# Performance work log

Measured on AMD Instinct MI355X. Metric: run time of the kernel, lower is better.

## Reference

```python
import jax, jax.numpy as jnp
import numpy as np
from functools import partial

EPS = 1e-8

@partial(jax.custom_vjp, nondiff_argnums=(2, 3))
def ste_quantize(x, scale, clamp_min, clamp_max):
    # forward: clamp(round(x/scale), min, max); backward: grad/scale (STE)
    return jnp.clip(jnp.round(x / scale), clamp_min, clamp_max)

def _ste_fwd(x, scale, clamp_min, clamp_max):
    return ste_quantize(x, scale, clamp_min, clamp_max), scale

def _ste_bwd(clamp_min, clamp_max, scale, g):
    return (g / scale, jnp.zeros_like(scale))

ste_quantize.defvjp(_ste_fwd, _ste_bwd)


def setup_inputs() -> dict:
    key = jax.random.key(0)
    kx, kw = jax.random.split(key)
    x = jax.random.normal(kx, (4, 4096, 2048), dtype=jnp.float32)
    # nn.init.normal_(weight, mean=0.0, std=0.006)
    weight = 0.006 * jax.random.normal(kw, (2048, 2048), dtype=jnp.float32)
    return {"x": x, "weight": weight}


def reference(x, weight):
    # per-tensor ternary weight quantization: alpha = mean(|W|)
    alpha = jnp.maximum(jnp.mean(jnp.abs(weight)), EPS)
    w_q = ste_quantize(weight, alpha, -1.0, 1.0)  # (out, in), values in {-1,0,1}
    # per-token int8 activation quantization: beta = max(|x|)/127
    beta = jnp.maximum(jnp.max(jnp.abs(x), axis=-1, keepdims=True) / 127.0, EPS)  # (b,s,1)
    x_q = ste_quantize(x, beta, -127.0, 127.0)  # (b,s,in)
    # fp32 GEMM on quantized values, then dequant rescale
    y = jnp.einsum('bsi,oi->bso', x_q, w_q)
    return y * alpha * beta
```

## Files before the change

kernel.cpp:

```cpp
#include <hip/hip_runtime.h>

#define IN_DIM 2048
#define OUT_DIM 2048
#define EPS 1e-8f

#define BM 256
#define BN 128
#define BK 64
#define NT (IN_DIM / BK)
#define SLOT 24576
#define LDS_SZ 73728

using int32x4 = __attribute__((ext_vector_type(4))) int;

__global__ __launch_bounds__(256) void absum_kernel(const float* __restrict__ w,
                                                    double* __restrict__ sum, int n4) {
    int tid = blockIdx.x * blockDim.x + threadIdx.x;
    int stride = gridDim.x * blockDim.x;
    float s = 0.f;
    for (int i = tid; i < n4; i += stride) {
        float4 v = ((const float4*)w)[i];
        s += fabsf(v.x) + fabsf(v.y) + fabsf(v.z) + fabsf(v.w);
    }
    for (int off = 32; off; off >>= 1) s += __shfl_down(s, off);
    __shared__ float wsum[4];
    int lane = threadIdx.x & 63, wave = threadIdx.x >> 6;
    if (lane == 0) wsum[wave] = s;
    __syncthreads();
    if (threadIdx.x == 0) {
        double t = (double)wsum[0] + (double)wsum[1] + (double)wsum[2] + (double)wsum[3];
        atomicAdd(sum, t);
    }
}

__global__ __launch_bounds__(256) void quantw_kernel(const float* __restrict__ w,
                                                     const double* __restrict__ sumptr,
                                                     signed char* __restrict__ wq,
                                                     float* __restrict__ alpha_out, int n4) {
    float alpha = fmaxf((float)(*sumptr * (1.0 / (double)(IN_DIM * OUT_DIM))), EPS);
    int i = blockIdx.x * blockDim.x + threadIdx.x;
    if (i == 0) *alpha_out = alpha;
    if (i >= n4) return;
    float4 v = ((const float4*)w)[i];
    char4 q;
    q.x = (signed char)fminf(fmaxf(rintf(v.x / alpha), -1.f), 1.f);
    q.y = (signed char)fminf(fmaxf(rintf(v.y / alpha), -1.f), 1.f);
    q.z = (signed char)fminf(fmaxf(rintf(v.z / alpha), -1.f), 1.f);
    q.w = (signed char)fminf(fmaxf(rintf(v.w / alpha), -1.f), 1.f);
    ((char4*)wq)[i] = q;
}

__global__ __launch_bounds__(256) void quantx_kernel(const float* __restrict__ x,
                                                     signed char* __restrict__ xq,
                                                     float* __restrict__ beta_arr,
                                                     int tokens) {
    const int tid = threadIdx.x;
    const int lane = tid & 63, wave = tid >> 6;
    __shared__ float wmax[4];
    for (int t = blockIdx.x; t < tokens; t += gridDim.x) {
        const float4* row = (const float4*)(x + (size_t)t * IN_DIM);
        float4 v0 = row[tid];
        float4 v1 = row[tid + 256];
        float m = fmaxf(fmaxf(fmaxf(fabsf(v0.x), fabsf(v0.y)), fmaxf(fabsf(v0.z), fabsf(v0.w))),
                        fmaxf(fmaxf(fabsf(v1.x), fabsf(v1.y)), fmaxf(fabsf(v1.z), fabsf(v1.w))));
        for (int off = 32; off; off >>= 1) m = fmaxf(m, __shfl_xor(m, off));
        if (lane == 0) wmax[wave] = m;
        __syncthreads();
        m = fmaxf(fmaxf(wmax[0], wmax[1]), fmaxf(wmax[2], wmax[3]));
        float beta = fmaxf(m * (1.f / 127.f), EPS);
        if (tid == 0) beta_arr[t] = beta;
        char4 q0, q1;
        q0.x = (signed char)fminf(fmaxf(rintf(v0.x / beta), -127.f), 127.f);
        q0.y = (signed char)fminf(fmaxf(rintf(v0.y / beta), -127.f), 127.f);
        q0.z = (signed char)fminf(fmaxf(rintf(v0.z / beta), -127.f), 127.f);
        q0.w = (signed char)fminf(fmaxf(rintf(v0.w / beta), -127.f), 127.f);
        q1.x = (signed char)fminf(fmaxf(rintf(v1.x / beta), -127.f), 127.f);
        q1.y = (signed char)fminf(fmaxf(rintf(v1.y / beta), -127.f), 127.f);
        q1.z = (signed char)fminf(fmaxf(rintf(v1.z / beta), -127.f), 127.f);
        q1.w = (signed char)fminf(fmaxf(rintf(v1.w / beta), -127.f), 127.f);
        char4* orow = (char4*)(xq + (size_t)t * IN_DIM);
        orow[tid] = q0;
        orow[tid + 256] = q1;
        __syncthreads();
    }
}

__device__ __forceinline__ void gll(const signed char* g, signed char* l) {
    __builtin_amdgcn_global_load_lds((const __attribute__((address_space(1))) void*)g,
        (__attribute__((address_space(3))) void*)l, 16, 0, 0);
}

__global__ __launch_bounds__(256, 2) void gemm_kernel(const signed char* __restrict__ xq,
                                                      const signed char* __restrict__ wq,
                                                      const float* __restrict__ beta,
                                                      const float* __restrict__ alpha_p,
                                                      float* __restrict__ out) {
    extern __shared__ signed char lds[];
    const int tid = threadIdx.x;
    const int lane = tid & 63;
    const int wave = tid >> 6;
    const int wm = wave >> 1;
    const int wn = wave & 1;
    const int col0 = blockIdx.x * BN;
    const int row0 = blockIdx.y * BM;

    const int f = tid * 16;
    const int srow = ((tid >> 6) << 4) + (tid & 15);
    const int skg = ((tid >> 4) & 3) << 4;
    const signed char* aP[4];
    const signed char* bP[2];
#pragma unroll
    for (int c = 0; c < 4; ++c) aP[c] = xq + (size_t)(row0 + srow + 64 * c) * IN_DIM + skg;
#pragma unroll
    for (int c = 0; c < 2; ++c) bP[c] = wq + (size_t)(col0 + srow + 64 * c) * IN_DIM + skg;

    const int kr = ((lane >> 4) << 8) + ((lane & 15) << 4);
    const int aoff = wm * 8192 + kr;
    const int boff = 16384 + wn * 4096 + kr;

    int32x4 acc[8][4] = {};

#pragma unroll
    for (int c = 0; c < 4; ++c) gll(aP[c], lds + f + c * 4096);
#pragma unroll
    for (int c = 0; c < 2; ++c) gll(bP[c], lds + 16384 + f + c * 4096);
#pragma unroll
    for (int c = 0; c < 4; ++c) gll(aP[c] + BK, lds + SLOT + f + c * 4096);
#pragma unroll
    for (int c = 0; c < 2; ++c) gll(bP[c] + BK, lds + SLOT + 16384 + f + c * 4096);
    asm volatile("s_waitcnt vmcnt(6)" ::: "memory");
    __builtin_amdgcn_s_barrier();

    int s = 0, d = 2;
    for (int T = 0; T < NT; ++T) {
        const signed char* ls = lds + s * SLOT;
        signed char* ldst = lds + d * SLOT;
        int32x4 af[8], bf[4];
#pragma unroll
        for (int m = 0; m < 4; ++m) af[m] = *(const int32x4*)(ls + aoff + m * 1024);
#pragma unroll
        for (int n = 0; n < 4; ++n) bf[n] = *(const int32x4*)(ls + boff + n * 1024);
        if (T < NT - 2) {
            const size_t ko = (size_t)(T + 2) * BK;
#pragma unroll
            for (int c = 0; c < 4; ++c) gll(aP[c] + ko, ldst + f + c * 4096);
        }
#pragma unroll
        for (int m = 0; m < 4; ++m) af[4 + m] = *(const int32x4*)(ls + aoff + 4096 + m * 1024);
        __builtin_amdgcn_s_setprio(1);
#pragma unroll
        for (int m = 0; m < 4; ++m)
#pragma unroll
            for (int n = 0; n < 4; ++n)
                acc[m][n] = __builtin_amdgcn_mfma_i32_16x16x64_i8(af[m], bf[n], acc[m][n], 0, 0, 0);
        __builtin_amdgcn_s_setprio(0);
        if (T < NT - 2) {
            const size_t ko = (size_t)(T + 2) * BK;
#pragma unroll
            for (int c = 0; c < 2; ++c) gll(bP[c] + ko, ldst + 16384 + f + c * 4096);
        }
        __builtin_amdgcn_s_setprio(1);
#pragma unroll
        for (int m = 0; m < 4; ++m)
#pragma unroll
            for (int n = 0; n < 4; ++n)
                acc[4 + m][n] = __builtin_amdgcn_mfma_i32_16x16x64_i8(af[4 + m], bf[n], acc[4 + m][n], 0, 0, 0);
        __builtin_amdgcn_s_setprio(0);
        if (T < NT - 1) {
            if (T < NT - 2) asm volatile("s_waitcnt vmcnt(6)" ::: "memory");
            else            asm volatile("s_waitcnt vmcnt(0)" ::: "memory");
            __builtin_amdgcn_s_barrier();
        }
        s = (s == 2) ? 0 : s + 1;
        d = (d == 2) ? 0 : d + 1;
    }

    const float alpha = *alpha_p;
#pragma unroll
    for (int mi = 0; mi < 8; ++mi) {
        int rbase = row0 + wm * 128 + mi * 16 + ((lane >> 4) << 2);
#pragma unroll
        for (int r = 0; r < 4; ++r) {
            int row = rbase + r;
            float scale = alpha * beta[row];
#pragma unroll
            for (int n = 0; n < 4; ++n) {
                int col = col0 + wn * 64 + n * 16 + (lane & 15);
                out[(size_t)row * OUT_DIM + col] = (float)acc[mi][n][r] * scale;
            }
        }
    }
}

extern "C" void kernel_launch(void* const* d_in, const int* in_sizes, int n_in,
                              void* d_out, int out_size, void* d_ws, size_t ws_size,
                              hipStream_t stream) {
    const float* x = (const float*)d_in[0];
    const float* w = (const float*)d_in[1];
    float* out = (float*)d_out;

    const int tokens = in_sizes[0] / IN_DIM;
    const int n_w = in_sizes[1];
    const int n_w4 = n_w / 4;

    char* ws = (char*)d_ws;
    double* d_sum = (double*)ws;
    float* d_alpha = (float*)(ws + 8);
    float* d_beta = (float*)(ws + 256);
    signed char* d_wq = (signed char*)(ws + 256 + 65536);
    signed char* d_xq = d_wq + (size_t)n_w;

    hipMemsetAsync(d_ws, 0, 16, stream);

    absum_kernel<<<1024, 256, 0, stream>>>(w, d_sum, n_w4);
    quantw_kernel<<<(n_w4 + 255) / 256, 256, 0, stream>>>(w, d_sum, d_wq, d_alpha, n_w4);
    quantx_kernel<<<2048, 256, 0, stream>>>(x, d_xq, d_beta, tokens);

    hipFuncSetAttribute((const void*)gemm_kernel,
                        hipFuncAttributeMaxDynamicSharedMemorySize, LDS_SZ);

    dim3 grid(OUT_DIM / BN, tokens / BM);
    gemm_kernel<<<grid, 256, LDS_SZ, stream>>>(d_xq, d_wq, d_beta, d_alpha, out);
}
```

Measured before the change: 172.0 us.

## Reshape GEMM tile to 128x256 with eight waves per block

Switches the int8 MFMA GEMM block tile from 256x128 with 4 waves to 128x256 with 8 waves. Each wave now computes a 64x64 sub-tile, which halves its accumulators, and the load addressing is rewritten so one A load and two B loads per thread fill the same LDS slot size. The intent is more waves per CU to hide latency. The trade-off is fewer MFMAs per LDS fragment read. Also, launch_bounds(512,4) asks for enough occupancy that the register budget may force spills.

Result: no change. 173.2 us (+0.7%).

```diff
diff --git a/kernel.cpp b/kernel.cpp
--- a/kernel.cpp
+++ b/kernel.cpp
@@ -4,8 +4,8 @@
 #define OUT_DIM 2048
 #define EPS 1e-8f
 
-#define BM 256
-#define BN 128
+#define BM 128
+#define BN 256
 #define BK 64
 #define NT (IN_DIM / BK)
 #define SLOT 24576
@@ -90,7 +90,7 @@
         (__attribute__((address_space(3))) void*)l, 16, 0, 0);
 }
 
-__global__ __launch_bounds__(256, 2) void gemm_kernel(const signed char* __restrict__ xq,
+__global__ __launch_bounds__(512, 4) void gemm_kernel(const signed char* __restrict__ xq,
                                                       const signed char* __restrict__ wq,
                                                       const float* __restrict__ beta,
                                                       const float* __restrict__ alpha_p,
@@ -99,76 +99,64 @@
     const int tid = threadIdx.x;
     const int lane = tid & 63;
     const int wave = tid >> 6;
-    const int wm = wave >> 1;
-    const int wn = wave & 1;
+    const int wm = wave >> 2;
+    const int wn = wave & 3;
     const int col0 = blockIdx.x * BN;
     const int row0 = blockIdx.y * BM;
 
     const int f = tid * 16;
     const int srow = ((tid >> 6) << 4) + (tid & 15);
     const int skg = ((tid >> 4) & 3) << 4;
-    const signed char* aP[4];
-    const signed char* bP[2];
-#pragma unroll
-    for (int c = 0; c < 4; ++c) aP[c] = xq + (size_t)(row0 + srow + 64 * c) * IN_DIM + skg;
-#pragma unroll
-    for (int c = 0; c < 2; ++c) bP[c] = wq + (size_t)(col0 + srow + 64 * c) * IN_DIM + skg;
+    const signed char* aP  = xq + (size_t)(row0 + srow) * IN_DIM + skg;
+    const signed char* b0P = wq + (size_t)(col0 + srow) * IN_DIM + skg;
+    const signed char* b1P = wq + (size_t)(col0 + 128 + srow) * IN_DIM + skg;
 
     const int kr = ((lane >> 4) << 8) + ((lane & 15) << 4);
-    const int aoff = wm * 8192 + kr;
-    const int boff = 16384 + wn * 4096 + kr;
-
-    int32x4 acc[8][4] = {};
-
-#pragma unroll
-    for (int c = 0; c < 4; ++c) gll(aP[c], lds + f + c * 4096);
-#pragma unroll
-    for (int c = 0; c < 2; ++c) gll(bP[c], lds + 16384 + f + c * 4096);
-#pragma unroll
-    for (int c = 0; c < 4; ++c) gll(aP[c] + BK, lds + SLOT + f + c * 4096);
-#pragma unroll
-    for (int c = 0; c < 2; ++c) gll(bP[c] + BK, lds + SLOT + 16384 + f + c * 4096);
-    asm volatile("s_waitcnt vmcnt(6)" ::: "memory");
+    const int aoff = (wm << 12) + kr;
+    const int boff = 8192 + (wn << 12) + kr;
+
+    int32x4 acc[4][4] = {};
+
+    gll(aP, lds + f);  gll(b0P, lds + 8192 + f);  gll(b1P, lds + 16384 + f);
+    gll(aP + BK, lds + SLOT + f);
+    gll(b0P + BK, lds + SLOT + 8192 + f);
+    gll(b1P + BK, lds + SLOT + 16384 + f);
+    asm volatile("s_waitcnt vmcnt(3)" ::: "memory");
     __builtin_amdgcn_s_barrier();
 
     int s = 0, d = 2;
     for (int T = 0; T < NT; ++T) {
         const signed char* ls = lds + s * SLOT;
         signed char* ldst = lds + d * SLOT;
-        int32x4 af[8], bf[4];
-#pragma unroll
-        for (int m = 0; m < 4; ++m) af[m] = *(const int32x4*)(ls + aoff + m * 1024);
+        const size_t ko = (size_t)(T + 2) * BK;
+        int32x4 af[4], bf[4];
+        af[0] = *(const int32x4*)(ls + aoff);
+        af[1] = *(const int32x4*)(ls + aoff + 1024);
 #pragma unroll
         for (int n = 0; n < 4; ++n) bf[n] = *(const int32x4*)(ls + boff + n * 1024);
-        if (T < NT - 2) {
-            const size_t ko = (size_t)(T + 2) * BK;
-#pragma unroll
-            for (int c = 0; c < 4; ++c) gll(aP[c] + ko, ldst + f + c * 4096);
-        }
-#pragma unroll
-        for (int m = 0; m < 4; ++m) af[4 + m] = *(const int32x4*)(ls + aoff + 4096 + m * 1024);
+        if (T < NT - 2) gll(aP + ko, ldst + f);
+        af[2] = *(const int32x4*)(ls + aoff + 2048);
+        af[3] = *(const int32x4*)(ls + aoff + 3072);
         __builtin_amdgcn_s_setprio(1);
 #pragma unroll
-        for (int m = 0; m < 4; ++m)
+        for (int m = 0; m < 2; ++m)
+#pragma unroll
+            for (int n = 0; n < 4; ++n)
+                acc[m][n] = __builtin_amdgcn_mfma_i32_16x16x64_i8(af[m], bf[n], acc[m][n], 0, 0, 0);
+        __builtin_amdgcn_s_setprio(0);
+        if (T < NT - 2) { gll(b0P + ko, ldst + 8192 + f); gll(b1P + ko, ldst + 16384 + f); }
+        __builtin_amdgcn_s_setprio(1);
+#pragma unroll
+        for (int m = 2; m < 4; ++m)
 #pragma unroll
             for (int n = 0; n < 4; ++n)
                 acc[m][n] = __builtin_amdgcn_mfma_i32_16x16x64_i8(af[m], bf[n], acc[m][n], 0, 0, 0);
         __builtin_amdgcn_s_setprio(0);
         if (T < NT - 2) {
-            const size_t ko = (size_t)(T + 2) * BK;
-#pragma unroll
-            for (int c = 0; c < 2; ++c) gll(bP[c] + ko, ldst + 16384 + f + c * 4096);
-        }
-        __builtin_amdgcn_s_setprio(1);
-#pragma unroll
-        for (int m = 0; m < 4; ++m)
-#pragma unroll
-            for (int n = 0; n < 4; ++n)
-                acc[4 + m][n] = __builtin_amdgcn_mfma_i32_16x16x64_i8(af[4 + m], bf[n], acc[4 + m][n], 0, 0, 0);
-        __builtin_amdgcn_s_setprio(0);
-        if (T < NT - 1) {
-            if (T < NT - 2) asm volatile("s_waitcnt vmcnt(6)" ::: "memory");
-            else            asm volatile("s_waitcnt vmcnt(0)" ::: "memory");
+            asm volatile("s_waitcnt vmcnt(3)" ::: "memory");
+            __builtin_amdgcn_s_barrier();
+        } else if (T == NT - 2) {
+            asm volatile("s_waitcnt vmcnt(0)" ::: "memory");
             __builtin_amdgcn_s_barrier();
         }
         s = (s == 2) ? 0 : s + 1;
@@ -177,8 +165,8 @@
 
     const float alpha = *alpha_p;
 #pragma unroll
-    for (int mi = 0; mi < 8; ++mi) {
-        int rbase = row0 + wm * 128 + mi * 16 + ((lane >> 4) << 2);
+    for (int mi = 0; mi < 4; ++mi) {
+        int rbase = row0 + wm * 64 + mi * 16 + ((lane >> 4) << 2);
 #pragma unroll
         for (int r = 0; r < 4; ++r) {
             int row = rbase + r;
@@ -220,5 +208,5 @@
                         hipFuncAttributeMaxDynamicSharedMemorySize, LDS_SZ);
 
     dim3 grid(OUT_DIM / BN, tokens / BM);
-    gemm_kernel<<<grid, 256, LDS_SZ, stream>>>(d_xq, d_wq, d_beta, d_alpha, out);
-}
+    gemm_kernel<<<grid, 512, LDS_SZ, stream>>>(d_xq, d_wq, d_beta, d_alpha, out);
+}
```
